# Performance work log

Measured on AMD Instinct MI355X. Metric: run time of the kernel, lower is better.

Reference implementation:

```python
import jax, jax.numpy as jnp
import numpy as np

NC = 80
NA = 3
BOX_GAIN, CLS_GAIN, OBJ_GAIN = 7.5, 0.5, 1.0
GAMMA = 1.5
LS = 0.0
EPS = 1e-7
ANCHORS = np.array([[[10, 13], [16, 30], [33, 23]],
                    [[30, 61], [62, 45], [59, 119]],
                    [[116, 90], [156, 198], [373, 326]]], dtype=np.float32)


def bce_logits(x, t):
    # numerically stable BCE-with-logits, elementwise
    return jnp.maximum(x, 0.0) - x * t + jnp.log1p(jnp.exp(-jnp.abs(x)))


def iou_cxcywh(b1, b2, eps=EPS):
    b1x1, b1x2 = b1[..., 0] - b1[..., 2] / 2, b1[..., 0] + b1[..., 2] / 2
    b1y1, b1y2 = b1[..., 1] - b1[..., 3] / 2, b1[..., 1] + b1[..., 3] / 2
    b2x1, b2x2 = b2[..., 0] - b2[..., 2] / 2, b2[..., 0] + b2[..., 2] / 2
    b2y1, b2y2 = b2[..., 1] - b2[..., 3] / 2, b2[..., 1] + b2[..., 3] / 2
    inter = jnp.clip(jnp.minimum(b1x2, b2x2) - jnp.maximum(b1x1, b2x1), 0.0) * \
            jnp.clip(jnp.minimum(b1y2, b2y2) - jnp.maximum(b1y1, b2y1), 0.0)
    w1, h1 = b1x2 - b1x1, b1y2 - b1y1 + eps
    w2, h2 = b2x2 - b2x1, b2y2 - b2y1 + eps
    union = w1 * h1 + w2 * h2 - inter + eps
    return inter / union


def _scale_loss(pred, targets, anchors):
    B, C, h, w = pred.shape
    p = pred.reshape(B, NA, NC + 5, h, w).transpose(0, 1, 3, 4, 2)  # [B,3,h,w,nc+5]
    pobj = p[..., 4]

    N = targets.shape[0]
    scale = jnp.array([w, h, w, h], dtype=pred.dtype)
    g = targets[:, 2:6] * scale  # grid-space cx,cy,w,h
    gx, gy = g[:, 0], g[:, 1]
    valid = (gx >= 0) & (gx < w) & (gy >= 0) & (gy < h)
    gi = jnp.clip(jnp.floor(gx).astype(jnp.int32), 0, w - 1)
    gj = jnp.clip(jnp.floor(gy).astype(jnp.int32), 0, h - 1)
    bidx = jnp.clip(targets[:, 0].astype(jnp.int32), 0, B - 1)
    cls = jnp.clip(targets[:, 1].astype(jnp.int32), 0, NC - 1)

    # each GT is assigned to all 3 anchors -> M = 3N rows
    rep = lambda v: jnp.repeat(v, NA, axis=0)
    bM, giM, gjM, clsM, maskM = rep(bidx), rep(gi), rep(gj), rep(cls), rep(valid)
    aiM = jnp.tile(jnp.arange(NA), N)
    anchM = anchors[aiM]                             # [M,2]
    txyM = rep(g[:, :2] - jnp.floor(g[:, :2]))       # cell-relative offsets
    twhM = rep(g[:, 2:4])
    mf = maskM.astype(pred.dtype)
    n_valid = mf.sum()

    # objectness target grid (duplicates collapse to 1 via max, like repeated set)
    tobj = jnp.zeros((B, NA, h, w), pred.dtype).at[bM, aiM, gjM, giM].max(mf)
    loss_obj = bce_logits(pobj, tobj).mean() * OBJ_GAIN

    ps = p[bM, aiM, gjM, giM]                        # [M, nc+5]
    ps_box, ps_cls = ps[:, :4], ps[:, 5:]

    # focal classification loss
    t = jax.nn.one_hot(clsM, NC, dtype=pred.dtype)
    if LS > 0:
        t = t * (1 - LS) + LS / NC
    ce = bce_logits(ps_cls, t)
    focal = (1.0 - jnp.exp(-ce)) ** GAMMA * ce       # [M, nc]
    row_sum = (focal * mf[:, None]).sum(-1)          # [M]
    loss_cls = jnp.where(n_valid > 0,
                         row_sum.sum() / (jnp.maximum(n_valid, 1.0) * NC),
                         0.0) * CLS_GAIN

    # per-class focal means (rows grouped by GT class)
    seg_ids = jnp.where(maskM, clsM, NC)
    seg_sum = jax.ops.segment_sum(row_sum, seg_ids, num_segments=NC + 1)[:NC]
    seg_cnt = jax.ops.segment_sum(mf, seg_ids, num_segments=NC + 1)[:NC]
    per_class = jnp.where(seg_cnt > 0,
                          seg_sum / (jnp.maximum(seg_cnt, 1.0) * NC),
                          0.0) * CLS_GAIN

    # box (IoU) loss
    pxy = jax.nn.sigmoid(ps_box[:, :2]) * 2.0 - 0.5
    pwh = (jax.nn.sigmoid(ps_box[:, 2:4]) * 2.0) ** 2 * anchM
    pbox = jnp.concatenate([pxy, pwh], axis=-1)
    tbox = jnp.concatenate([txyM, twhM], axis=-1)
    iou = iou_cxcywh(pbox, tbox)
    loss_box = jnp.where(n_valid > 0,
                         ((1.0 - iou) * mf).sum() / jnp.maximum(n_valid, 1.0),
                         0.0) * BOX_GAIN

    return loss_box, loss_cls, loss_obj, per_class


def setup_inputs() -> dict:
    key = jax.random.key(0)
    k0, k1, k2, kb, kc, kxy, kwh = jax.random.split(key, 7)
    B, N = 16, 800
    p0 = jax.random.normal(k0, (B, NA * (NC + 5), 80, 80), jnp.float32)
    p1 = jax.random.normal(k1, (B, NA * (NC + 5), 40, 40), jnp.float32)
    p2 = jax.random.normal(k2, (B, NA * (NC + 5), 20, 20), jnp.float32)
    bcol = jax.random.randint(kb, (N, 1), 0, B).astype(jnp.float32)
    ccol = jax.random.randint(kc, (N, 1), 0, NC).astype(jnp.float32)
    xy = jax.random.uniform(kxy, (N, 2), jnp.float32, 0.02, 0.98)
    wh = jax.random.uniform(kwh, (N, 2), jnp.float32, 0.02, 0.30)
    targets = jnp.concatenate([bcol, ccol, xy, wh], axis=1)  # [N,6]
    return {"p0": p0, "p1": p1, "p2": p2, "targets": targets}


def reference(p0, p1, p2, targets):
    anchors = jnp.asarray(ANCHORS)
    lb = lc = lo = 0.0
    pc = jnp.zeros((NC,), jnp.float32)
    for i, pred in enumerate((p0, p1, p2)):
        b, c, o, per_class = _scale_loss(pred, targets, anchors[i])
        lb, lc, lo = lb + b, lc + c, lo + o
        pc = pc + per_class
    total = lb + lc + lo
    # [loss, loss_box, loss_cls, loss_obj, per-class cls losses...]
    return jnp.concatenate([jnp.stack([total, lb, lc, lo]), pc])
```

## Files before the change

kernel.cpp:

```cpp
#include <hip/hip_runtime.h>
#include <math.h>

#define NC 80
#define TCOLS 6

__device__ __constant__ float c_anch[3][3][2] = {
  {{10.f,13.f},{16.f,30.f},{33.f,23.f}},
  {{30.f,61.f},{62.f,45.f},{59.f,119.f}},
  {{116.f,90.f},{156.f,198.f},{373.f,326.f}}
};

#define ACC_CORR   0
#define ACC_BOX(s) (16 + 16*(s))
#define ACC_CLS(s) (64 + 16*(s))
#define ACC_NV(s)  (112 + 16*(s))
#define ACC_SEG    160
#define ACC_TOTAL  (160 + 6*NC)

#define OBJ_BLOCKS 61
#define HSIZE 4096

__device__ __forceinline__ float bce0(float x) {
  return fmaxf(x, 0.f) + log1pf(expf(-fabsf(x)));
}
__device__ __forceinline__ float bce(float x, float t) {
  return fmaxf(x, 0.f) - x * t + log1pf(expf(-fabsf(x)));
}
__device__ __forceinline__ float focal(float x, float t) {
  float ce = bce(x, t);
  float u  = 1.f - expf(-ce);
  return u * sqrtf(u) * ce;
}

__global__ void k_init(float* __restrict__ acc) {
  for (int k = threadIdx.x; k < ACC_TOTAL; k += blockDim.x) acc[k] = 0.f;
}

__global__ __launch_bounds__(1024, 8)
void k_fused(const float* __restrict__ p0, const float* __restrict__ p1,
             const float* __restrict__ p2, const float* __restrict__ tgt,
             int N, int B, int RB, float* __restrict__ acc,
             float* __restrict__ partial) {
  const int bid = blockIdx.x;
  const int tid = threadIdx.x;

  if (bid < RB) {
    __shared__ float l_box[3], l_cls[3], l_nv[3];
    if (tid < 3) { l_box[tid]=0.f; l_cls[tid]=0.f; l_nv[tid]=0.f; }
    __syncthreads();
    int row   = bid * 16 + (tid >> 6);
    int lane  = tid & 63;
    int nrows = 3 * N * 3;
    if (row < nrows) {
      int rps = N * 3;
      int s   = row / rps;
      int rem = row - s * rps;
      int n   = rem / 3;
      int a   = rem - n * 3;
      int w   = (s == 0) ? 80 : ((s == 1) ? 40 : 20);
      int hw  = w * w;
      const float* pred = (s == 0) ? p0 : ((s == 1) ? p1 : p2);
      float fw = (float)w;
      float gx = tgt[n*TCOLS + 2] * fw, gy = tgt[n*TCOLS + 3] * fw;
      if (gx >= 0.f && gx < fw && gy >= 0.f && gy < fw) {
        float gw = tgt[n*TCOLS + 4] * fw, gh = tgt[n*TCOLS + 5] * fw;
        int gi  = min(max((int)floorf(gx), 0), w - 1);
        int gj  = min(max((int)floorf(gy), 0), w - 1);
        int b   = min(max((int)tgt[n*TCOLS + 0], 0), B - 1);
        int cls = min(max((int)tgt[n*TCOLS + 1], 0), NC - 1);
        size_t base = (size_t)(b*255 + a*85) * hw + (size_t)(gj*w + gi);

        float x0  = pred[base + (size_t)(5 + lane) * hw];
        float x1  = pred[base + (size_t)(69 + (lane & 15)) * hw];
        float bxv = (lane < 4) ? pred[base + (size_t)lane * hw] : 0.f;

        float rs = focal(x0, (lane == cls) ? 1.f : 0.f);
        if (lane < 16) rs += focal(x1, ((64 + lane) == cls) ? 1.f : 0.f);
        for (int off = 32; off > 0; off >>= 1) rs += __shfl_xor(rs, off, 64);

        float bx = __shfl(bxv, 0, 64), by = __shfl(bxv, 1, 64);
        float bw = __shfl(bxv, 2, 64), bh = __shfl(bxv, 3, 64);
        if (lane == 0) {
          float sx = 1.f/(1.f + expf(-bx));
          float sy = 1.f/(1.f + expf(-by));
          float sw = 1.f/(1.f + expf(-bw));
          float sh = 1.f/(1.f + expf(-bh));
          float px = sx*2.f - 0.5f, py = sy*2.f - 0.5f;
          float aw = c_anch[s][a][0], ah = c_anch[s][a][1];
          float pw = (sw*2.f)*(sw*2.f)*aw, ph = (sh*2.f)*(sh*2.f)*ah;
          float txf = gx - floorf(gx), tyf = gy - floorf(gy);
          float b1x1 = px - pw*0.5f, b1x2 = px + pw*0.5f;
          float b1y1 = py - ph*0.5f, b1y2 = py + ph*0.5f;
          float b2x1 = txf - gw*0.5f, b2x2 = txf + gw*0.5f;
          float b2y1 = tyf - gh*0.5f, b2y2 = tyf + gh*0.5f;
          float iw = fmaxf(fminf(b1x2, b2x2) - fmaxf(b1x1, b2x1), 0.f);
          float ih = fmaxf(fminf(b1y2, b2y2) - fmaxf(b1y1, b2y1), 0.f);
          float inter = iw * ih;
          float w1 = b1x2 - b1x1, h1 = b1y2 - b1y1 + 1e-7f;
          float w2 = b2x2 - b2x1, h2 = b2y2 - b2y1 + 1e-7f;
          float uni = w1*h1 + w2*h2 - inter + 1e-7f;
          float iou = inter / uni;

          atomicAdd(&l_box[s], 1.f - iou);
          atomicAdd(&l_cls[s], rs);
          atomicAdd(&l_nv[s],  1.f);
          atomicAdd(&acc[ACC_SEG +        s*NC + cls], rs);
          atomicAdd(&acc[ACC_SEG + 3*NC + s*NC + cls], 1.f);
        }
      }
    }
    __syncthreads();
    if (tid < 3) {
      int s = tid; float v;
      v = l_box[s]; if (v != 0.f) atomicAdd(&acc[ACC_BOX(s)], v);
      v = l_cls[s]; if (v != 0.f) atomicAdd(&acc[ACC_CLS(s)], v);
      v = l_nv [s]; if (v != 0.f) atomicAdd(&acc[ACC_NV (s)], v);
    }
  } else if (bid < RB + OBJ_BLOCKS) {
    const int ob = bid - RB;
    const int n0 = B*3*6400, n1 = B*3*1600, n2 = B*3*400;
    const int total4 = (n0 + n1 + n2) >> 2;
    const float i0 = 1.f/(float)n0, i1 = 1.f/(float)n1, i2 = 1.f/(float)n2;
    float local = 0.f;
    for (int i = ob * 1024 + tid; i < total4; i += OBJ_BLOCKS * 1024) {
      int e = i << 2;
      const float* pred; int idx, hw; float inv;
      if (e < n0)         { pred = p0; idx = e;           hw = 6400; inv = i0; }
      else if (e < n0+n1) { pred = p1; idx = e - n0;      hw = 1600; inv = i1; }
      else                { pred = p2; idx = e - n0 - n1; hw = 400;  inv = i2; }
      int ba = idx / hw, pix = idx - ba * hw;
      int b = ba / 3, a = ba - b * 3;
      const float4 x4 = *(const float4*)&pred[(size_t)(b*255 + a*85 + 4) * hw + pix];
      local += (bce0(x4.x) + bce0(x4.y) + bce0(x4.z) + bce0(x4.w)) * inv;
    }
    for (int off = 32; off > 0; off >>= 1) local += __shfl_xor(local, off, 64);
    __shared__ float red[16];
    if ((tid & 63) == 0) red[tid >> 6] = local;
    __syncthreads();
    if (tid == 0) {
      float t = 0.f;
      for (int k = 0; k < 16; ++k) t += red[k];
      partial[ob] = t;
    }
  } else {
    __shared__ int htab[HSIZE];
    __shared__ float cred[16];
    for (int k = tid; k < HSIZE; k += 1024) htab[k] = -1;
    __syncthreads();
    int M = 3 * N;
    float corr = 0.f;
    for (int i = tid; i < M; i += 1024) {
      int s = i / N, n = i - s * N;
      int w = (s == 0) ? 80 : ((s == 1) ? 40 : 20);
      float fw = (float)w;
      float gx = tgt[n*TCOLS + 2] * fw, gy = tgt[n*TCOLS + 3] * fw;
      if (gx >= 0.f && gx < fw && gy >= 0.f && gy < fw) {
        int hw = w * w;
        int gi = min(max((int)floorf(gx), 0), w - 1);
        int gj = min(max((int)floorf(gy), 0), w - 1);
        int b  = min(max((int)tgt[n*TCOLS + 0], 0), B - 1);
        int idx = b * hw + gj * w + gi;
        int key = (s << 17) | idx;
        unsigned h = ((unsigned)key * 2654435761u) >> 20;
        bool owner = false;
        for (;;) {
          int old = atomicCAS(&htab[h & (HSIZE-1)], -1, key);
          if (old == -1)  { owner = true; break; }
          if (old == key) { break; }
          ++h;
        }
        if (owner) {
          const float* pred = (s == 0) ? p0 : ((s == 1) ? p1 : p2);
          int cell = idx - b * hw;
          float inv = 1.f / (float)(B * 3 * hw);
          float sum = pred[(size_t)(b*255 +   4) * hw + cell]
                    + pred[(size_t)(b*255 +  89) * hw + cell]
                    + pred[(size_t)(b*255 + 174) * hw + cell];
          corr -= sum * inv;
        }
      }
    }
    for (int off = 32; off > 0; off >>= 1) corr += __shfl_xor(corr, off, 64);
    if ((tid & 63) == 0) cred[tid >> 6] = corr;
    __syncthreads();
    if (tid == 0) {
      float t = 0.f;
      for (int k = 0; k < 16; ++k) t += cred[k];
      acc[ACC_CORR] = t;
    }
  }
}

__global__ void k_final(const float* __restrict__ acc, const float* __restrict__ partial,
                        float* __restrict__ out) {
  __shared__ float slo;
  int t = threadIdx.x;
  float v = (t < OBJ_BLOCKS) ? partial[t] : 0.f;
  for (int off = 32; off > 0; off >>= 1) v += __shfl_xor(v, off, 64);
  if (t == 0) slo = v;
  __syncthreads();
  if (t == 0) {
    float lo = slo + acc[ACC_CORR];
    float lb = 0.f, lc = 0.f;
    for (int s = 0; s < 3; ++s) {
      float nv  = acc[ACC_NV(s)];
      float nvm = fmaxf(nv, 1.f);
      if (nv > 0.f) {
        lb += acc[ACC_BOX(s)] / nvm * 7.5f;
        lc += acc[ACC_CLS(s)] / (nvm * (float)NC) * 0.5f;
      }
    }
    out[0] = lb + lc + lo;
    out[1] = lb;
    out[2] = lc;
    out[3] = lo;
  }
  if (t < NC) {
    float pc = 0.f;
    for (int s = 0; s < 3; ++s) {
      float cnt = acc[ACC_SEG + 3*NC + s*NC + t];
      if (cnt > 0.f)
        pc += acc[ACC_SEG + s*NC + t] / (fmaxf(cnt, 1.f) * (float)NC) * 0.5f;
    }
    out[4 + t] = pc;
  }
}

extern "C" void kernel_launch(void* const* d_in, const int* in_sizes, int n_in,
                              void* d_out, int out_size, void* d_ws, size_t ws_size,
                              hipStream_t stream) {
  const float* p0  = (const float*)d_in[0];
  const float* p1  = (const float*)d_in[1];
  const float* p2  = (const float*)d_in[2];
  const float* tgt = (const float*)d_in[3];
  int N = in_sizes[3] / TCOLS;
  int B = in_sizes[0] / (255 * 6400);
  float* out = (float*)d_out;

  float* acc     = (float*)d_ws;
  float* partial = acc + ACC_TOTAL;

  int nrows = 3 * N * 3;
  int RB = (nrows + 15) / 16;

  k_init <<<1, 256, 0, stream>>>(acc);
  k_fused<<<RB + OBJ_BLOCKS + 1, 1024, 0, stream>>>(p0, p1, p2, tgt, N, B, RB, acc, partial);
  k_final<<<1, 128, 0, stream>>>(acc, partial, out);
}
```

Before: 41.19 us.

## Fold final reduction into main kernel via last-block ticket, use fast math

Drops the separate init and finalize kernels. A memset zeroes the accumulators, and the last block to finish, found through an atomic ticket counter, computes the outputs inside the fused kernel. Objectness partials now go straight into a global atomic accumulator. The object block count drops from 61 to 31, and each block handles 15 rows instead of 16. Fast intrinsic exp, log and sqrt replace the precise versions, which cuts launch overhead and math cost but may slightly change numerical accuracy.

Measured after the change: 52.14 us. +26.6%, slower.

```diff
diff --git a/kernel.cpp b/kernel.cpp
--- a/kernel.cpp
+++ b/kernel.cpp
@@ -3,6 +3,9 @@
 
 #define NC 80
 #define TCOLS 6
+#define OBJB 31
+#define HSIZE 4096
+#define RPB 15
 
 __device__ __constant__ float c_anch[3][3][2] = {
   {{10.f,13.f},{16.f,30.f},{33.f,23.f}},
@@ -10,48 +13,48 @@
   {{116.f,90.f},{156.f,198.f},{373.f,326.f}}
 };
 
-#define ACC_CORR   0
-#define ACC_BOX(s) (16 + 16*(s))
-#define ACC_CLS(s) (64 + 16*(s))
-#define ACC_NV(s)  (112 + 16*(s))
-#define ACC_SEG    160
-#define ACC_TOTAL  (160 + 6*NC)
-
-#define OBJ_BLOCKS 61
-#define HSIZE 4096
-
-__device__ __forceinline__ float bce0(float x) {
-  return fmaxf(x, 0.f) + log1pf(expf(-fabsf(x)));
-}
-__device__ __forceinline__ float bce(float x, float t) {
-  return fmaxf(x, 0.f) - x * t + log1pf(expf(-fabsf(x)));
-}
-__device__ __forceinline__ float focal(float x, float t) {
-  float ce = bce(x, t);
-  float u  = 1.f - expf(-ce);
-  return u * sqrtf(u) * ce;
-}
-
-__global__ void k_init(float* __restrict__ acc) {
-  for (int k = threadIdx.x; k < ACC_TOTAL; k += blockDim.x) acc[k] = 0.f;
+#define ACC_OBJ    0
+#define ACC_CORR   16
+#define ACC_BOX(s) (32 + 16*(s))
+#define ACC_CLS(s) (80 + 16*(s))
+#define ACC_NV(s)  (128 + 16*(s))
+#define ACC_SEG    176
+#define ACC_TICKET 672
+#define ACC_TOTAL  688
+
+__device__ __forceinline__ float fbce0(float x) {
+  return fmaxf(x, 0.f) + __logf(1.f + __expf(-fabsf(x)));
+}
+__device__ __forceinline__ float fbce(float x, float t) {
+  return fmaxf(x, 0.f) - x * t + __logf(1.f + __expf(-fabsf(x)));
+}
+__device__ __forceinline__ float ffocal(float x, float t) {
+  float ce = fbce(x, t);
+  float u  = 1.f - __expf(-ce);
+  return u * __builtin_amdgcn_sqrtf(u) * ce;
 }
 
 __global__ __launch_bounds__(1024, 8)
-void k_fused(const float* __restrict__ p0, const float* __restrict__ p1,
-             const float* __restrict__ p2, const float* __restrict__ tgt,
-             int N, int B, int RB, float* __restrict__ acc,
-             float* __restrict__ partial) {
+void k_all(const float* __restrict__ p0, const float* __restrict__ p1,
+           const float* __restrict__ p2, const float* __restrict__ tgt,
+           int N, int B, int RB, float* __restrict__ acc,
+           float* __restrict__ out) {
   const int bid = blockIdx.x;
   const int tid = threadIdx.x;
 
+  __shared__ int   htab[HSIZE];
+  __shared__ float l_box[3], l_cls[3], l_nv[3];
+  __shared__ float red[16];
+  __shared__ unsigned s_rank;
+
   if (bid < RB) {
-    __shared__ float l_box[3], l_cls[3], l_nv[3];
     if (tid < 3) { l_box[tid]=0.f; l_cls[tid]=0.f; l_nv[tid]=0.f; }
     __syncthreads();
-    int row   = bid * 16 + (tid >> 6);
-    int lane  = tid & 63;
-    int nrows = 3 * N * 3;
-    if (row < nrows) {
+    int wv   = tid >> 6;
+    int lane = tid & 63;
+    int row  = bid * RPB + wv;
+    int nrows = 9 * N;
+    if (wv < RPB && row < nrows) {
       int rps = N * 3;
       int s   = row / rps;
       int rem = row - s * rps;
@@ -74,17 +77,17 @@
         float x1  = pred[base + (size_t)(69 + (lane & 15)) * hw];
         float bxv = (lane < 4) ? pred[base + (size_t)lane * hw] : 0.f;
 
-        float rs = focal(x0, (lane == cls) ? 1.f : 0.f);
-        if (lane < 16) rs += focal(x1, ((64 + lane) == cls) ? 1.f : 0.f);
+        float rs = ffocal(x0, (lane == cls) ? 1.f : 0.f);
+        if (lane < 16) rs += ffocal(x1, ((64 + lane) == cls) ? 1.f : 0.f);
         for (int off = 32; off > 0; off >>= 1) rs += __shfl_xor(rs, off, 64);
 
         float bx = __shfl(bxv, 0, 64), by = __shfl(bxv, 1, 64);
         float bw = __shfl(bxv, 2, 64), bh = __shfl(bxv, 3, 64);
         if (lane == 0) {
-          float sx = 1.f/(1.f + expf(-bx));
-          float sy = 1.f/(1.f + expf(-by));
-          float sw = 1.f/(1.f + expf(-bw));
-          float sh = 1.f/(1.f + expf(-bh));
+          float sx = 1.f/(1.f + __expf(-bx));
+          float sy = 1.f/(1.f + __expf(-by));
+          float sw = 1.f/(1.f + __expf(-bw));
+          float sh = 1.f/(1.f + __expf(-bh));
           float px = sx*2.f - 0.5f, py = sy*2.f - 0.5f;
           float aw = c_anch[s][a][0], ah = c_anch[s][a][1];
           float pw = (sw*2.f)*(sw*2.f)*aw, ph = (sh*2.f)*(sh*2.f)*ah;
@@ -116,13 +119,13 @@
       v = l_cls[s]; if (v != 0.f) atomicAdd(&acc[ACC_CLS(s)], v);
       v = l_nv [s]; if (v != 0.f) atomicAdd(&acc[ACC_NV (s)], v);
     }
-  } else if (bid < RB + OBJ_BLOCKS) {
+  } else if (bid < RB + OBJB) {
     const int ob = bid - RB;
     const int n0 = B*3*6400, n1 = B*3*1600, n2 = B*3*400;
     const int total4 = (n0 + n1 + n2) >> 2;
     const float i0 = 1.f/(float)n0, i1 = 1.f/(float)n1, i2 = 1.f/(float)n2;
     float local = 0.f;
-    for (int i = ob * 1024 + tid; i < total4; i += OBJ_BLOCKS * 1024) {
+    for (int i = ob * 1024 + tid; i < total4; i += OBJB * 1024) {
       int e = i << 2;
       const float* pred; int idx, hw; float inv;
       if (e < n0)         { pred = p0; idx = e;           hw = 6400; inv = i0; }
@@ -131,20 +134,17 @@
       int ba = idx / hw, pix = idx - ba * hw;
       int b = ba / 3, a = ba - b * 3;
       const float4 x4 = *(const float4*)&pred[(size_t)(b*255 + a*85 + 4) * hw + pix];
-      local += (bce0(x4.x) + bce0(x4.y) + bce0(x4.z) + bce0(x4.w)) * inv;
+      local += (fbce0(x4.x) + fbce0(x4.y) + fbce0(x4.z) + fbce0(x4.w)) * inv;
     }
     for (int off = 32; off > 0; off >>= 1) local += __shfl_xor(local, off, 64);
-    __shared__ float red[16];
     if ((tid & 63) == 0) red[tid >> 6] = local;
     __syncthreads();
     if (tid == 0) {
       float t = 0.f;
       for (int k = 0; k < 16; ++k) t += red[k];
-      partial[ob] = t;
+      atomicAdd(&acc[ACC_OBJ], t);
     }
   } else {
-    __shared__ int htab[HSIZE];
-    __shared__ float cred[16];
     for (int k = tid; k < HSIZE; k += 1024) htab[k] = -1;
     __syncthreads();
     int M = 3 * N;
@@ -181,33 +181,34 @@
       }
     }
     for (int off = 32; off > 0; off >>= 1) corr += __shfl_xor(corr, off, 64);
-    if ((tid & 63) == 0) cred[tid >> 6] = corr;
+    if ((tid & 63) == 0) red[tid >> 6] = corr;
     __syncthreads();
     if (tid == 0) {
       float t = 0.f;
-      for (int k = 0; k < 16; ++k) t += cred[k];
-      acc[ACC_CORR] = t;
-    }
-  }
-}
-
-__global__ void k_final(const float* __restrict__ acc, const float* __restrict__ partial,
-                        float* __restrict__ out) {
-  __shared__ float slo;
-  int t = threadIdx.x;
-  float v = (t < OBJ_BLOCKS) ? partial[t] : 0.f;
-  for (int off = 32; off > 0; off >>= 1) v += __shfl_xor(v, off, 64);
-  if (t == 0) slo = v;
+      for (int k = 0; k < 16; ++k) t += red[k];
+      atomicAdd(&acc[ACC_CORR], t);
+    }
+  }
+
   __syncthreads();
-  if (t == 0) {
-    float lo = slo + acc[ACC_CORR];
+  if (tid == 0) {
+    __threadfence();
+    s_rank = atomicAdd((unsigned int*)&acc[ACC_TICKET], 1u);
+  }
+  __syncthreads();
+  if (s_rank != (unsigned)(gridDim.x - 1)) return;
+
+  __threadfence();
+  #define AL(i) atomicAdd(&acc[(i)], 0.0f)
+  if (tid == 0) {
+    float lo = AL(ACC_OBJ) + AL(ACC_CORR);
     float lb = 0.f, lc = 0.f;
     for (int s = 0; s < 3; ++s) {
-      float nv  = acc[ACC_NV(s)];
+      float nv  = AL(ACC_NV(s));
       float nvm = fmaxf(nv, 1.f);
       if (nv > 0.f) {
-        lb += acc[ACC_BOX(s)] / nvm * 7.5f;
-        lc += acc[ACC_CLS(s)] / (nvm * (float)NC) * 0.5f;
+        lb += AL(ACC_BOX(s)) / nvm * 7.5f;
+        lc += AL(ACC_CLS(s)) / (nvm * (float)NC) * 0.5f;
       }
     }
     out[0] = lb + lc + lo;
@@ -215,15 +216,16 @@
     out[2] = lc;
     out[3] = lo;
   }
-  if (t < NC) {
+  if (tid < NC) {
     float pc = 0.f;
     for (int s = 0; s < 3; ++s) {
-      float cnt = acc[ACC_SEG + 3*NC + s*NC + t];
+      float cnt = AL(ACC_SEG + 3*NC + s*NC + tid);
       if (cnt > 0.f)
-        pc += acc[ACC_SEG + s*NC + t] / (fmaxf(cnt, 1.f) * (float)NC) * 0.5f;
-    }
-    out[4 + t] = pc;
-  }
+        pc += AL(ACC_SEG + s*NC + tid) / (fmaxf(cnt, 1.f) * (float)NC) * 0.5f;
+    }
+    out[4 + tid] = pc;
+  }
+  #undef AL
 }
 
 extern "C" void kernel_launch(void* const* d_in, const int* in_sizes, int n_in,
@@ -236,14 +238,12 @@
   int N = in_sizes[3] / TCOLS;
   int B = in_sizes[0] / (255 * 6400);
   float* out = (float*)d_out;
-
-  float* acc     = (float*)d_ws;
-  float* partial = acc + ACC_TOTAL;
-
-  int nrows = 3 * N * 3;
-  int RB = (nrows + 15) / 16;
-
-  k_init <<<1, 256, 0, stream>>>(acc);
-  k_fused<<<RB + OBJ_BLOCKS + 1, 1024, 0, stream>>>(p0, p1, p2, tgt, N, B, RB, acc, partial);
-  k_final<<<1, 128, 0, stream>>>(acc, partial, out);
-}
+  float* acc = (float*)d_ws;
+
+  int nrows = 9 * N;
+  int RB = (nrows + RPB - 1) / RPB;
+  int grid = RB + OBJB + 1;
+
+  hipMemsetAsync(acc, 0, ACC_TOTAL * sizeof(float), stream);
+  k_all<<<grid, 1024, 0, stream>>>(p0, p1, p2, tgt, N, B, RB, acc, out);
+}
```
